# Optimization experiments

Measured on AMD Instinct MI355X. Metric: run time of the kernel, lower is better.

Reference implementation:

```python
import jax, jax.numpy as jnp
import numpy as np

H, W = 16, 16  # input_resolution
NUM_HEADS = 16
DIM = 512


def build_relative_position_index(h, w):
    coords = np.stack(np.meshgrid(np.arange(h), np.arange(w), indexing='ij'))  # [2,h,w]
    cf = coords.reshape(2, -1)
    rel = cf[:, :, None] - cf[:, None, :]            # [2,N,N]
    rel = rel.transpose(1, 2, 0).astype(np.int32)    # [N,N,2]
    rel[:, :, 0] += h - 1
    rel[:, :, 1] += w - 1
    rel[:, :, 0] *= 2 * w - 1
    return jnp.asarray(rel.sum(-1).reshape(-1), dtype=jnp.int32)  # [N*N]


def setup_inputs() -> dict:
    key = jax.random.key(0)
    ks = jax.random.split(key, 6)
    B, N, C = 128, H * W, DIM
    x = jax.random.normal(ks[0], (B, N, C), dtype=jnp.float32)
    qkv_w = jax.random.normal(ks[1], (3 * C, C), dtype=jnp.float32) * (C ** -0.5)
    qkv_b = jax.random.normal(ks[2], (3 * C,), dtype=jnp.float32) * 0.02
    proj_w = jax.random.normal(ks[3], (C, C), dtype=jnp.float32) * (C ** -0.5)
    proj_b = jax.random.normal(ks[4], (C,), dtype=jnp.float32) * 0.02
    bias_table = jax.random.normal(ks[5], ((2 * H - 1) * (2 * W - 1), NUM_HEADS), dtype=jnp.float32) * 0.02
    rel_index = build_relative_position_index(H, W)
    return {"x": x, "qkv_w": qkv_w, "qkv_b": qkv_b, "proj_w": proj_w,
            "proj_b": proj_b, "bias_table": bias_table, "rel_index": rel_index}


def reference(x, qkv_w, qkv_b, proj_w, proj_b, bias_table, rel_index):
    B, N, C = x.shape
    h = NUM_HEADS
    hd = C // h
    scale = hd ** -0.5
    # qkv projection: [B,N,3C] -> [3,B,h,N,hd]
    qkv = (jnp.einsum('bnc,oc->bno', x, qkv_w) + qkv_b)
    qkv = qkv.reshape(B, N, 3, h, hd).transpose(2, 0, 3, 1, 4)
    q, k, v = qkv[0], qkv[1], qkv[2]
    # relative position bias: gather [N*N,h] -> [1,h,N,N]
    bias = bias_table[rel_index].reshape(N, N, h).transpose(2, 0, 1)[None]
    attn = jnp.einsum('bhnd,bhmd->bhnm', q * scale, k) + bias
    attn = jax.nn.softmax(attn, axis=-1)
    out = jnp.einsum('bhnm,bhmd->bhnd', attn, v)     # [B,h,N,hd]
    out = out.transpose(0, 2, 1, 3).reshape(B, N, C)
    return jnp.einsum('bnc,oc->bno', out, proj_w) + proj_b
```

## Files before the change

kernel.cpp:

```cpp
#include <hip/hip_runtime.h>

typedef __bf16 bf16_t;
typedef __bf16 bf16x8 __attribute__((ext_vector_type(8)));
typedef float f32x4 __attribute__((ext_vector_type(4)));

#define MFMA_16x16x32(a, b, c) __builtin_amdgcn_mfma_f32_16x16x32_bf16((a), (b), (c), 0, 0, 0)

__device__ inline bf16x8 cvt8(const float* __restrict__ p) {
  bf16x8 r;
#pragma unroll
  for (int j = 0; j < 8; j++) r[j] = (bf16_t)p[j];
  return r;
}

__device__ inline void load_lds16(const bf16_t* g, bf16_t* l) {
  __builtin_amdgcn_global_load_lds(
      (const __attribute__((address_space(1))) void*)g,
      (__attribute__((address_space(3))) void*)l, 16, 0, 0);
}

__global__ __launch_bounds__(256) void convert_k(
    const float* __restrict__ x, const float* __restrict__ qkv_w,
    const float* __restrict__ proj_w,
    bf16_t* __restrict__ xbf, bf16_t* __restrict__ wqkvbf,
    bf16_t* __restrict__ wprojbf) {
  size_t base = ((size_t)blockIdx.x * 256 + threadIdx.x) * 8;
  if (base < 16777216) {
    *(bf16x8*)(xbf + base) = cvt8(x + base);
  } else if (base < 17563648) {
    size_t o = base - 16777216;
    *(bf16x8*)(wqkvbf + o) = cvt8(qkv_w + o);
  } else {
    size_t o = base - 17563648;
    *(bf16x8*)(wprojbf + o) = cvt8(proj_w + o);
  }
}

__global__ __launch_bounds__(256) void bias_gather_k(
    const float* __restrict__ table, const int* __restrict__ rel,
    float* __restrict__ biasws) {
  int idx = blockIdx.x * 256 + threadIdx.x;
  int h = idx >> 16;
  int rem = idx & 65535;
  int rb = rem >> 12;
  int ct = (rem >> 8) & 15;
  int L = (rem >> 2) & 63;
  int r = idx & 3;
  int row = rb * 16 + (L >> 4) * 4 + r;
  int col = ct * 16 + (L & 15);
  biasws[idx] = table[rel[row * 256 + col] * 16 + h];
}

#define PH_OPEN() __builtin_amdgcn_s_setprio(1)

#define PH_CLOSE()                                        \
  do {                                                    \
    __builtin_amdgcn_s_setprio(0);                        \
    asm volatile("s_waitcnt lgkmcnt(0)" ::: "memory");    \
    __builtin_amdgcn_sched_barrier(0);                    \
    __builtin_amdgcn_s_barrier();                         \
    __builtin_amdgcn_sched_barrier(0);                    \
  } while (0)

#define GATE4()                                           \
  do {                                                    \
    __builtin_amdgcn_s_setprio(0);                        \
    asm volatile("s_waitcnt vmcnt(4)" ::: "memory");      \
    __builtin_amdgcn_s_barrier();                         \
    __builtin_amdgcn_sched_barrier(0);                    \
  } while (0)

#define GATE0()                                           \
  do {                                                    \
    __builtin_amdgcn_s_setprio(0);                        \
    asm volatile("s_waitcnt vmcnt(0)" ::: "memory");      \
    __builtin_amdgcn_s_barrier();                         \
    __builtin_amdgcn_sched_barrier(0);                    \
  } while (0)

#define STG2(src, dst, c)                                                        \
  do {                                                                           \
    load_lds16((src) + (c)*32768, (dst) + (c)*4096);                             \
    load_lds16((src) + ((c) + 1) * 32768, (dst) + ((c) + 1) * 4096);             \
  } while (0)

#define RDA(dst, buf, ibase)                                                     \
  _Pragma("unroll") for (int i = 0; i < 4; ++i) {                                \
    dst[i][0] = *(const bf16x8*)&As[(buf)*16384 + a0 + ((ibase) + i) * 1024];    \
    dst[i][1] = *(const bf16x8*)&As[(buf)*16384 + a1 + ((ibase) + i) * 1024];    \
  }
#define RDB(dst, buf, jbase)                                                     \
  _Pragma("unroll") for (int j = 0; j < 2; ++j) {                                \
    dst[j][0] = *(const bf16x8*)&Bs[(buf)*16384 + b0 + ((jbase) + j) * 1024];    \
    dst[j][1] = *(const bf16x8*)&Bs[(buf)*16384 + b1 + ((jbase) + j) * 1024];    \
  }

#define MFQ(Af, Bf, I0, J0)                                                      \
  _Pragma("unroll") for (int i = 0; i < 4; ++i) _Pragma("unroll")                \
      for (int j = 0; j < 2; ++j) {                                              \
    acc[(I0) + i][(J0) + j] =                                                    \
        MFMA_16x16x32(Af[i][0], Bf[j][0], acc[(I0) + i][(J0) + j]);              \
    acc[(I0) + i][(J0) + j] =                                                    \
        MFMA_16x16x32(Af[i][1], Bf[j][1], acc[(I0) + i][(J0) + j]);              \
  }

#define GEMM_SETUP(Ap, Wp)                                                       \
  __shared__ bf16_t As[2 * 16384];                                               \
  __shared__ bf16_t Bs[2 * 16384];                                               \
  const int t = threadIdx.x;                                                     \
  const int w = t >> 6, L = t & 63;                                              \
  const int wm = w >> 2, wn = w & 3;                                             \
  const int lrow = L & 15, lq = L >> 4;                                          \
  const int srow = t >> 3;                                                       \
  const int sslot = (t & 7) ^ (srow & 7);                                        \
  const bf16_t* ga = (Ap) + (size_t)(m0 + srow) * 512 + sslot * 8;               \
  const bf16_t* gb = (Wp) + (size_t)(n0 + srow) * 512 + sslot * 8;               \
  bf16_t* la = As + t * 8;                                                       \
  bf16_t* lb = Bs + t * 8;                                                       \
  const int m8 = (lrow & 7) * 8;                                                 \
  const int a0 = (wm * 128 + lrow) * 64 + ((lq * 8) ^ m8);                       \
  const int a1 = (wm * 128 + lrow) * 64 + ((32 + lq * 8) ^ m8);                  \
  const int b0 = (wn * 64 + lrow) * 64 + ((lq * 8) ^ m8);                        \
  const int b1 = (wn * 64 + lrow) * 64 + ((32 + lq * 8) ^ m8);

#define PROLOGUE()                                                               \
  STG2(ga, la, 0); STG2(ga, la, 2);                                              \
  STG2(gb, lb, 0); STG2(gb, lb, 2);                                              \
  STG2(ga + 64, la + 16384, 0); STG2(ga + 64, la + 16384, 2);                    \
  asm volatile("s_waitcnt vmcnt(4)" ::: "memory");                               \
  __builtin_amdgcn_s_barrier();                                                  \
  __builtin_amdgcn_sched_barrier(0);

#define HALF_STEADY(CUR, LBDST, LADST, GBP, GAP)                                 \
  {                                                                              \
    bf16x8 fal[4][2], fbl[2][2], fah[4][2], fbh[2][2];                           \
                                                                        \
    RDA(fal, CUR, 0); RDB(fbl, CUR, 0); RDB(fbh, CUR, 2);                        \
    STG2(GBP, LBDST, 0);                                                         \
    PH_OPEN(); MFQ(fal, fbl, 0, 0); PH_CLOSE();                                  \
                                                                        \
    RDA(fah, CUR, 4);                                                            \
    STG2(GBP, LBDST, 2);                                                         \
    PH_OPEN(); MFQ(fal, fbh, 0, 2); PH_CLOSE();                                  \
                                                                        \
    STG2(GAP, LADST, 0);                                                         \
    PH_OPEN(); MFQ(fah, fbh, 4, 2); PH_CLOSE();                                  \
                                                                        \
    STG2(GAP, LADST, 2);                                                         \
    PH_OPEN(); MFQ(fah, fbl, 4, 0); GATE4();                                     \
  }

#define GEMM_LOOP()                                                              \
  {                                                                              \
    const bf16_t* gA = ga + 128;                                       \
    const bf16_t* gB = gb + 64;                                        \
    _Pragma("unroll 1") for (int G = 0; G < 3; ++G) {                            \
      HALF_STEADY(0, lb + 16384, la, gB, gA)                                     \
      HALF_STEADY(1, lb, la + 16384, gB + 64, gA + 64)                           \
      gA += 128; gB += 128;                                                      \
    }                                                                            \
    {            \
      bf16x8 fal[4][2], fbl[2][2], fah[4][2], fbh[2][2];                         \
      RDA(fal, 0, 0); RDB(fbl, 0, 0); RDB(fbh, 0, 2);                            \
      STG2(gB, lb + 16384, 0);                                                   \
      PH_OPEN(); MFQ(fal, fbl, 0, 0); PH_CLOSE();                                \
      RDA(fah, 0, 4);                                                            \
      STG2(gB, lb + 16384, 2);                                                   \
      PH_OPEN(); MFQ(fal, fbh, 0, 2); PH_CLOSE();                                \
      PH_OPEN(); MFQ(fah, fbh, 4, 2); PH_CLOSE();                                \
      PH_OPEN(); MFQ(fah, fbl, 4, 0); GATE0();                                   \
    }                                                                            \
    {                               \
      bf16x8 fal[4][2], fbl[2][2], fah[4][2], fbh[2][2];                         \
      RDA(fal, 1, 0); RDB(fbl, 1, 0); RDB(fbh, 1, 2);                            \
      PH_OPEN(); MFQ(fal, fbl, 0, 0); PH_CLOSE();                                \
      RDA(fah, 1, 4);                                                            \
      PH_OPEN(); MFQ(fal, fbh, 0, 2); PH_CLOSE();                                \
      PH_OPEN(); MFQ(fah, fbh, 4, 2); PH_CLOSE();                                \
      PH_OPEN(); MFQ(fah, fbl, 4, 0);                                            \
      __builtin_amdgcn_s_setprio(0);                                             \
      __builtin_amdgcn_sched_barrier(0);                                         \
    }                                                                            \
  }

__global__ __launch_bounds__(512, 2) void qkv_gemm256_k(
    const bf16_t* __restrict__ A, const bf16_t* __restrict__ W,
    const float* __restrict__ Bvec,
    bf16_t* __restrict__ qws, bf16_t* __restrict__ kws, bf16_t* __restrict__ vws) {
  const int id = blockIdx.x;
  const int wg = (id & 7) * 96 + (id >> 3);
  const int mt = wg / 6, nt = wg % 6;
  const int m0 = mt * 256, n0 = nt * 256;

  GEMM_SETUP(A, W);

  f32x4 acc[8][4];
#pragma unroll
  for (int jj = 0; jj < 4; ++jj) {
    float bv = Bvec[n0 + wn * 64 + jj * 16 + lrow];
#pragma unroll
    for (int i = 0; i < 8; ++i) acc[i][jj] = (f32x4){bv, bv, bv, bv};
  }

  PROLOGUE();
  GEMM_LOOP();

  const int col0 = n0 + wn * 64;
  const int s = col0 >> 9;
  bf16_t* dst = (s == 0) ? qws : (s == 1) ? kws : vws;
  const float mul = (s == 0) ? 0.17677669529663687f : 1.0f;
#pragma unroll
  for (int jj = 0; jj < 4; ++jj) {
    int o = col0 + jj * 16 + lrow;
    int rem = o & 511;
    int hh = rem >> 5, d = rem & 31;
#pragma unroll
    for (int i = 0; i < 8; ++i) {
#pragma unroll
      for (int r = 0; r < 4; ++r) {
        int m = m0 + wm * 128 + i * 16 + lq * 4 + r;
        int b = m >> 8, n = m & 255;
        dst[(size_t)(((b * 16 + hh) * 256 + n) << 5) + d] =
            (bf16_t)(acc[i][jj][r] * mul);
      }
    }
  }
}

__global__ __launch_bounds__(512, 2) void proj_gemm256_k(
    const bf16_t* __restrict__ A, const bf16_t* __restrict__ W,
    const float* __restrict__ Bvec, float* __restrict__ out) {
  const int id = blockIdx.x;
  const int lin = (id & 7) * 32 + (id >> 3);
  const int mt = lin >> 1, nt = lin & 1;
  const int m0 = mt * 256, n0 = nt * 256;

  GEMM_SETUP(A, W);

  f32x4 acc[8][4];
#pragma unroll
  for (int jj = 0; jj < 4; ++jj) {
    float bv = Bvec[n0 + wn * 64 + jj * 16 + lrow];
#pragma unroll
    for (int i = 0; i < 8; ++i) acc[i][jj] = (f32x4){bv, bv, bv, bv};
  }

  PROLOGUE();
  GEMM_LOOP();

#pragma unroll
  for (int jj = 0; jj < 4; ++jj) {
    int o = n0 + wn * 64 + jj * 16 + lrow;
#pragma unroll
    for (int i = 0; i < 8; ++i) {
#pragma unroll
      for (int r = 0; r < 4; ++r) {
        int m = m0 + wm * 128 + i * 16 + lq * 4 + r;
        out[(size_t)m * 512 + o] = acc[i][jj][r];
      }
    }
  }
}

__global__ __launch_bounds__(256) void attn_k(
    const bf16_t* __restrict__ qws, const bf16_t* __restrict__ kws,
    const bf16_t* __restrict__ vws, const float* __restrict__ biasws,
    bf16_t* __restrict__ aows) {
  __shared__ __align__(16) char smem[33792 + 16896];
  bf16_t* Ps = (bf16_t*)smem;
  bf16_t* Vs = (bf16_t*)(smem + 33792);

  const int id = blockIdx.x;
  const int xcd = id & 7;
  const int jj = id >> 3;
  const int bh = (jj >> 2) * 8 + xcd;
  const int strip = jj & 3;
  const int h = bh & 15, b = bh >> 4;

  const int t = threadIdx.x;
  const int w = t >> 6, L = t & 63;
  const int lrow = L & 15, lq = L >> 4;

  const bf16_t* kbase = kws + (size_t)bh * 8192;
  const bf16_t* vbase = vws + (size_t)bh * 8192;
#pragma unroll
  for (int c = 0; c < 4; c++) {
    bf16x8 vv = *(const bf16x8*)(vbase + t * 32 + c * 8);
#pragma unroll
    for (int j = 0; j < 8; j++) Vs[(c * 8 + j) * 264 + t] = vv[j];
  }

  const bf16_t* qbase = qws + (size_t)bh * 8192 + (strip * 64 + w * 16) * 32;
  bf16x8 qf = *(const bf16x8*)(qbase + lrow * 32 + lq * 8);
  bf16x8 kf[16];
#pragma unroll
  for (int ct = 0; ct < 16; ct++)
    kf[ct] = *(const bf16x8*)(kbase + (ct * 16 + lrow) * 32 + lq * 8);

  const float* bb = biasws + h * 65536 + (strip * 4 + w) * 4096;
  f32x4 S[16];
#pragma unroll
  for (int ct = 0; ct < 16; ct++) {
    f32x4 bi = *(const f32x4*)(bb + ct * 256 + L * 4);
    S[ct] = MFMA_16x16x32(qf, kf[ct], bi);
  }

  float sm[4] = {0.f, 0.f, 0.f, 0.f};
#pragma unroll
  for (int ct = 0; ct < 16; ct++)
#pragma unroll
    for (int r = 0; r < 4; r++) {
      float e = __expf(S[ct][r]);
      S[ct][r] = e;
      sm[r] += e;
    }
#pragma unroll
  for (int r = 0; r < 4; r++)
#pragma unroll
    for (int msk = 1; msk < 16; msk <<= 1)
      sm[r] += __shfl_xor(sm[r], msk, 64);
  float inv[4];
#pragma unroll
  for (int r = 0; r < 4; r++) inv[r] = 1.0f / sm[r];

  bf16_t* Pw = Ps + w * 4224;
#pragma unroll
  for (int ct = 0; ct < 16; ct++)
#pragma unroll
    for (int r = 0; r < 4; r++)
      Pw[(lq * 4 + r) * 264 + ct * 16 + lrow] = (bf16_t)S[ct][r];

  __syncthreads();

  f32x4 O0 = {}, O1 = {};
#pragma unroll
  for (int c = 0; c < 8; c++) {
    bf16x8 pf = *(const bf16x8*)&Pw[lrow * 264 + c * 32 + lq * 8];
    bf16x8 v0 = *(const bf16x8*)&Vs[lrow * 264 + c * 32 + lq * 8];
    bf16x8 v1 = *(const bf16x8*)&Vs[(16 + lrow) * 264 + c * 32 + lq * 8];
    O0 = MFMA_16x16x32(pf, v0, O0);
    O1 = MFMA_16x16x32(pf, v1, O1);
  }
  bf16_t* obase = aows + (size_t)(b * 256 + strip * 64 + w * 16) * 512 + h * 32;
#pragma unroll
  for (int r = 0; r < 4; r++) {
    int rl = lq * 4 + r;
    obase[rl * 512 + lrow] = (bf16_t)(O0[r] * inv[r]);
    obase[rl * 512 + 16 + lrow] = (bf16_t)(O1[r] * inv[r]);
  }
}

extern "C" void kernel_launch(void* const* d_in, const int* in_sizes, int n_in,
                              void* d_out, int out_size, void* d_ws, size_t ws_size,
                              hipStream_t stream) {
  (void)in_sizes; (void)n_in; (void)out_size; (void)ws_size;
  const float* x      = (const float*)d_in[0];
  const float* qkv_w  = (const float*)d_in[1];
  const float* qkv_b  = (const float*)d_in[2];
  const float* proj_w = (const float*)d_in[3];
  const float* proj_b = (const float*)d_in[4];
  const float* table  = (const float*)d_in[5];
  const int*   rel    = (const int*)d_in[6];

  const size_t QKV_ELEMS = 16777216;
  bf16_t* qws     = (bf16_t*)d_ws;
  bf16_t* kws     = qws + QKV_ELEMS;
  bf16_t* vws     = kws + QKV_ELEMS;
  float*  biasws  = (float*)(vws + QKV_ELEMS);
  bf16_t* wqkvbf  = (bf16_t*)(biasws + 1048576);
  bf16_t* wprojbf = wqkvbf + 786432;
  bf16_t* xbf     = wprojbf + 262144;
  bf16_t* aows    = xbf;
  float*  out     = (float*)d_out;

  convert_k<<<8704, 256, 0, stream>>>(x, qkv_w, proj_w, xbf, wqkvbf, wprojbf);
  bias_gather_k<<<4096, 256, 0, stream>>>(table, rel, biasws);
  qkv_gemm256_k<<<768, 512, 0, stream>>>(xbf, wqkvbf, qkv_b, qws, kws, vws);
  attn_k<<<8192, 256, 0, stream>>>(qws, kws, vws, biasws, aows);
  proj_gemm256_k<<<256, 512, 0, stream>>>(aows, wprojbf, proj_b, out);
}
```

Measured before the change: 291.4 us.

## Compute transposed scores and pass P to PV MFMA via ds_bpermute instead of LDS

The attention kernel now computes S^T (K as the A operand), so each lane holds one query column. Row sums then need only two cross-lane shuffles, and normalization happens before the bf16 pack. The probability tile is rearranged into the PV operand layout with ds_bpermute rather than a round trip through LDS. Each block now handles a whole (batch, head) and loops over four query strips per wave, so V is staged in LDS once per head. The bias gather layout is transposed to match. The trade-offs are fewer blocks and K being reloaded from global in every strip iteration.

```diff
diff --git a/kernel.cpp b/kernel.cpp
--- a/kernel.cpp
+++ b/kernel.cpp
@@ -42,13 +42,13 @@
   int idx = blockIdx.x * 256 + threadIdx.x;
   int h = idx >> 16;
   int rem = idx & 65535;
-  int rb = rem >> 12;
+  int qb = rem >> 12;
   int ct = (rem >> 8) & 15;
   int L = (rem >> 2) & 63;
   int r = idx & 3;
-  int row = rb * 16 + (L >> 4) * 4 + r;
-  int col = ct * 16 + (L & 15);
-  biasws[idx] = table[rel[row * 256 + col] * 16 + h];
+  int q = qb * 16 + (L & 15);
+  int k = ct * 16 + (L >> 4) * 4 + r;
+  biasws[idx] = table[rel[q * 256 + k] * 16 + h];
 }
 
 #define PH_OPEN() __builtin_amdgcn_s_setprio(1)
@@ -134,18 +134,14 @@
 #define HALF_STEADY(CUR, LBDST, LADST, GBP, GAP)                                 \
   {                                                                              \
     bf16x8 fal[4][2], fbl[2][2], fah[4][2], fbh[2][2];                           \
-                                                                        \
     RDA(fal, CUR, 0); RDB(fbl, CUR, 0); RDB(fbh, CUR, 2);                        \
     STG2(GBP, LBDST, 0);                                                         \
     PH_OPEN(); MFQ(fal, fbl, 0, 0); PH_CLOSE();                                  \
-                                                                        \
     RDA(fah, CUR, 4);                                                            \
     STG2(GBP, LBDST, 2);                                                         \
     PH_OPEN(); MFQ(fal, fbh, 0, 2); PH_CLOSE();                                  \
-                                                                        \
     STG2(GAP, LADST, 0);                                                         \
     PH_OPEN(); MFQ(fah, fbh, 4, 2); PH_CLOSE();                                  \
-                                                                        \
     STG2(GAP, LADST, 2);                                                         \
     PH_OPEN(); MFQ(fah, fbl, 4, 0); GATE4();                                     \
   }
@@ -266,15 +262,9 @@
     const bf16_t* __restrict__ qws, const bf16_t* __restrict__ kws,
     const bf16_t* __restrict__ vws, const float* __restrict__ biasws,
     bf16_t* __restrict__ aows) {
-  __shared__ __align__(16) char smem[33792 + 16896];
-  bf16_t* Ps = (bf16_t*)smem;
-  bf16_t* Vs = (bf16_t*)(smem + 33792);
-
-  const int id = blockIdx.x;
-  const int xcd = id & 7;
-  const int jj = id >> 3;
-  const int bh = (jj >> 2) * 8 + xcd;
-  const int strip = jj & 3;
+  __shared__ __align__(16) bf16_t Vs[32 * 264];
+
+  const int bh = blockIdx.x;
   const int h = bh & 15, b = bh >> 4;
 
   const int t = threadIdx.x;
@@ -283,70 +273,92 @@
 
   const bf16_t* kbase = kws + (size_t)bh * 8192;
   const bf16_t* vbase = vws + (size_t)bh * 8192;
+
 #pragma unroll
   for (int c = 0; c < 4; c++) {
     bf16x8 vv = *(const bf16x8*)(vbase + t * 32 + c * 8);
 #pragma unroll
     for (int j = 0; j < 8; j++) Vs[(c * 8 + j) * 264 + t] = vv[j];
   }
-
-  const bf16_t* qbase = qws + (size_t)bh * 8192 + (strip * 64 + w * 16) * 32;
-  bf16x8 qf = *(const bf16x8*)(qbase + lrow * 32 + lq * 8);
-  bf16x8 kf[16];
-#pragma unroll
-  for (int ct = 0; ct < 16; ct++)
-    kf[ct] = *(const bf16x8*)(kbase + (ct * 16 + lrow) * 32 + lq * 8);
-
-  const float* bb = biasws + h * 65536 + (strip * 4 + w) * 4096;
-  f32x4 S[16];
-#pragma unroll
-  for (int ct = 0; ct < 16; ct++) {
-    f32x4 bi = *(const f32x4*)(bb + ct * 256 + L * 4);
-    S[ct] = MFMA_16x16x32(qf, kf[ct], bi);
-  }
-
-  float sm[4] = {0.f, 0.f, 0.f, 0.f};
-#pragma unroll
-  for (int ct = 0; ct < 16; ct++)
+  __syncthreads();
+
+  const int idxA = ((2 * (lq & 1)) * 16 + lrow) * 4;
+  const int idxB = idxA + 64;
+  const bool gsel = (lq < 2);
+
+  const float* bbw = biasws + h * 65536 + (w * 4) * 4096;
+
+#pragma unroll 1
+  for (int s = 0; s < 4; ++s) {
+    const int qrow0 = w * 64 + s * 16;
+    const bf16_t* qbase = qws + (size_t)bh * 8192 + qrow0 * 32;
+    bf16x8 qf = *(const bf16x8*)(qbase + lrow * 32 + lq * 8);
+    const float* bb = bbw + s * 4096;
+
+    f32x4 S[16];
+#pragma unroll
+    for (int ct = 0; ct < 16; ct++) {
+      bf16x8 kf = *(const bf16x8*)(kbase + (ct * 16 + lrow) * 32 + lq * 8);
+      f32x4 bi = *(const f32x4*)(bb + ct * 256 + L * 4);
+      S[ct] = MFMA_16x16x32(kf, qf, bi);
+    }
+
+    float sm = 0.f;
+#pragma unroll
+    for (int ct = 0; ct < 16; ct++)
+#pragma unroll
+      for (int r = 0; r < 4; r++) {
+        float e = __expf(S[ct][r]);
+        S[ct][r] = e;
+        sm += e;
+      }
+    sm += __shfl_xor(sm, 16, 64);
+    sm += __shfl_xor(sm, 32, 64);
+    const float inv = 1.0f / sm;
+
+    int pd[16][2];
+#pragma unroll
+    for (int ct = 0; ct < 16; ct++) {
+#pragma unroll
+      for (int j = 0; j < 2; j++) {
+        float lo = S[ct][2 * j] * inv;
+        float hi = S[ct][2 * j + 1] * inv;
+        int d;
+        asm("v_cvt_pk_bf16_f32 %0, %1, %2" : "=v"(d) : "v"(lo), "v"(hi));
+        pd[ct][j] = d;
+      }
+    }
+
+    f32x4 O0 = {}, O1 = {};
+#pragma unroll
+    for (int kt = 0; kt < 8; kt++) {
+      int rA0 = __builtin_amdgcn_ds_bpermute(idxA, pd[2 * kt][0]);
+      int rA1 = __builtin_amdgcn_ds_bpermute(idxA, pd[2 * kt][1]);
+      int rA2 = __builtin_amdgcn_ds_bpermute(idxB, pd[2 * kt][0]);
+      int rA3 = __builtin_amdgcn_ds_bpermute(idxB, pd[2 * kt][1]);
+      int rB0 = __builtin_amdgcn_ds_bpermute(idxA, pd[2 * kt + 1][0]);
+      int rB1 = __builtin_amdgcn_ds_bpermute(idxA, pd[2 * kt + 1][1]);
+      int rB2 = __builtin_amdgcn_ds_bpermute(idxB, pd[2 * kt + 1][0]);
+      int rB3 = __builtin_amdgcn_ds_bpermute(idxB, pd[2 * kt + 1][1]);
+      int4 Di;
+      Di.x = gsel ? rA0 : rB0;
+      Di.y = gsel ? rA1 : rB1;
+      Di.z = gsel ? rA2 : rB2;
+      Di.w = gsel ? rA3 : rB3;
+      bf16x8 pf = *reinterpret_cast<bf16x8*>(&Di);
+      bf16x8 v0 = *(const bf16x8*)&Vs[lrow * 264 + kt * 32 + lq * 8];
+      bf16x8 v1 = *(const bf16x8*)&Vs[(16 + lrow) * 264 + kt * 32 + lq * 8];
+      O0 = MFMA_16x16x32(pf, v0, O0);
+      O1 = MFMA_16x16x32(pf, v1, O1);
+    }
+
+    bf16_t* obase = aows + (size_t)(b * 256 + qrow0) * 512 + h * 32;
 #pragma unroll
     for (int r = 0; r < 4; r++) {
-      float e = __expf(S[ct][r]);
-      S[ct][r] = e;
-      sm[r] += e;
-    }
-#pragma unroll
-  for (int r = 0; r < 4; r++)
-#pragma unroll
-    for (int msk = 1; msk < 16; msk <<= 1)
-      sm[r] += __shfl_xor(sm[r], msk, 64);
-  float inv[4];
-#pragma unroll
-  for (int r = 0; r < 4; r++) inv[r] = 1.0f / sm[r];
-
-  bf16_t* Pw = Ps + w * 4224;
-#pragma unroll
-  for (int ct = 0; ct < 16; ct++)
-#pragma unroll
-    for (int r = 0; r < 4; r++)
-      Pw[(lq * 4 + r) * 264 + ct * 16 + lrow] = (bf16_t)S[ct][r];
-
-  __syncthreads();
-
-  f32x4 O0 = {}, O1 = {};
-#pragma unroll
-  for (int c = 0; c < 8; c++) {
-    bf16x8 pf = *(const bf16x8*)&Pw[lrow * 264 + c * 32 + lq * 8];
-    bf16x8 v0 = *(const bf16x8*)&Vs[lrow * 264 + c * 32 + lq * 8];
-    bf16x8 v1 = *(const bf16x8*)&Vs[(16 + lrow) * 264 + c * 32 + lq * 8];
-    O0 = MFMA_16x16x32(pf, v0, O0);
-    O1 = MFMA_16x16x32(pf, v1, O1);
-  }
-  bf16_t* obase = aows + (size_t)(b * 256 + strip * 64 + w * 16) * 512 + h * 32;
-#pragma unroll
-  for (int r = 0; r < 4; r++) {
-    int rl = lq * 4 + r;
-    obase[rl * 512 + lrow] = (bf16_t)(O0[r] * inv[r]);
-    obase[rl * 512 + 16 + lrow] = (bf16_t)(O1[r] * inv[r]);
+      int rl = lq * 4 + r;
+      obase[rl * 512 + lrow] = (bf16_t)(O0[r]);
+      obase[rl * 512 + 16 + lrow] = (bf16_t)(O1[r]);
+    }
   }
 }
 
@@ -376,6 +388,6 @@
   convert_k<<<8704, 256, 0, stream>>>(x, qkv_w, proj_w, xbf, wqkvbf, wprojbf);
   bias_gather_k<<<4096, 256, 0, stream>>>(table, rel, biasws);
   qkv_gemm256_k<<<768, 512, 0, stream>>>(xbf, wqkvbf, qkv_b, qws, kws, vws);
-  attn_k<<<8192, 256, 0, stream>>>(qws, kws, vws, biasws, aows);
+  attn_k<<<2048, 256, 0, stream>>>(qws, kws, vws, biasws, aows);
   proj_gemm256_k<<<256, 512, 0, stream>>>(aows, wprojbf, proj_b, out);
 }
```

Result: no change. 295.8 us (+1.5%).
